# Performance work log

Hardware: AMD Instinct MI355X
Metric: run time of the kernel (lower is better)

The kernel has to match this reference:

```python
import jax, jax.numpy as jnp
import numpy as np

B, IN, OUT, STY = 8192, 2048, 2048, 512

def setup_inputs() -> dict:
    key = jax.random.key(0)
    k1, k2, k3, k4, k5 = jax.random.split(key, 5)
    bound_w = 1.0 / np.sqrt(IN)  # kaiming_uniform(a=sqrt(5)) on (OUT,IN) -> U(-1/sqrt(IN), 1/sqrt(IN))
    weight = jax.random.uniform(k1, (OUT, IN), jnp.float32, -bound_w, bound_w)
    bias = jax.random.uniform(k2, (OUT,), jnp.float32, -bound_w, bound_w)
    bound_a = 1.0 / np.sqrt(STY)
    aff_w = jax.random.uniform(k3, (2 * OUT, STY), jnp.float32, -bound_a, bound_a)
    aff_b = jnp.concatenate([jnp.ones((OUT,), jnp.float32), jnp.zeros((OUT,), jnp.float32)])
    inp = jax.random.normal(k4, (B, IN), jnp.float32)
    style = jax.random.normal(k5, (B, STY), jnp.float32)
    return {"input": inp, "style": style, "weight": weight, "bias": bias,
            "aff_w": aff_w, "aff_b": aff_b}

def reference(input, style, weight, bias, aff_w, aff_b):
    # affine: (B, 2*OUT), chunk into scale / (unused) style-bias
    enc = style @ aff_w.T + aff_b
    scale = enc[:, :OUT]  # (B, OUT); second chunk is discarded by the original forward
    # Original math: w1 = W * s[b,o]; norm = rsqrt(sum_i w1^2); w2 = w1 / norm = w1 * sqrt(sum_i w1^2)
    # sum_i (W[o,i]*s[b,o])^2 = s[b,o]^2 * rowsq[o]  ->  w2[b,o,i] = W[o,i] * s*|s| * sqrt(rowsq[o])
    rowsq = jnp.sum(weight * weight, axis=1)                  # (OUT,)
    mod = scale * jnp.abs(scale) * jnp.sqrt(rowsq)[None, :]   # (B, OUT)
    base = input @ weight.T                                   # (B, OUT) single GEMM
    return base * mod + bias[None, :]
```

## Files before the change

kernel.cpp:

```cpp
#include <hip/hip_runtime.h>
#include <cstdint>
#include <cstddef>

#define B_ROWS 8192
#define IN_DIM 2048
#define OUT_DIM 2048
#define STY_DIM 512

typedef unsigned short u16;
typedef __attribute__((ext_vector_type(8))) short bf16x8;
typedef __attribute__((ext_vector_type(4))) float f32x4;

__device__ __forceinline__ void cvt_pair(float x0, float x1, uint32_t& hi, uint32_t& lo) {
  uint32_t u0 = __float_as_uint(x0), u1 = __float_as_uint(x1);
  uint32_t a0 = u0 & 0xffff0000u, a1 = u1 & 0xffff0000u;
  hi = (u0 >> 16) | a1;
  float l0 = x0 - __uint_as_float(a0);
  float l1 = x1 - __uint_as_float(a1);
  lo = (__float_as_uint(l0) >> 16) | (__float_as_uint(l1) & 0xffff0000u);
}


__global__ void split_kernel(const float* __restrict__ src,
                             u16* __restrict__ hi, u16* __restrict__ lo, int n4) {
  int stride = gridDim.x * blockDim.x;
  for (int i = blockIdx.x * blockDim.x + threadIdx.x; i < n4; i += stride) {
    float4 v = reinterpret_cast<const float4*>(src)[i];
    uint32_t h0, h1, l0, l1;
    cvt_pair(v.x, v.y, h0, l0);
    cvt_pair(v.z, v.w, h1, l1);
    uint2 hw; hw.x = h0; hw.y = h1;
    uint2 lw; lw.x = l0; lw.y = l1;
    reinterpret_cast<uint2*>(hi)[i] = hw;
    reinterpret_cast<uint2*>(lo)[i] = lw;
  }
}

__global__ void rowsq_kernel(const float* __restrict__ w, float* __restrict__ srq) {
  int row  = blockIdx.x * 4 + (threadIdx.x >> 6);
  int lane = threadIdx.x & 63;
  const float4* p = reinterpret_cast<const float4*>(w + (size_t)row * IN_DIM);
  float s = 0.f;
  #pragma unroll
  for (int i = 0; i < 8; ++i) {
    float4 v = p[lane + i * 64];
    s += v.x * v.x + v.y * v.y + v.z * v.z + v.w * v.w;
  }
  #pragma unroll
  for (int off = 32; off > 0; off >>= 1) s += __shfl_down(s, off);
  if (lane == 0) srq[row] = sqrtf(s);
}

template<int LDK, int NT>
__device__ __forceinline__ void gemm_bf16_phase(
    const u16* __restrict__ gAhi, const u16* __restrict__ gAlo,
    const u16* __restrict__ gBhi, const u16* __restrict__ gBlo,
    f32x4 (&acc)[4][4],
    u16* sAhi, u16* sAlo, u16* sBhi, u16* sBlo,
    int tid)
{
  const int lane = tid & 63;
  const int wid  = tid >> 6;
  const int wr = wid >> 1, wc = wid & 1;
  const int fr = lane & 15, kg = lane >> 4;

  const u16* gsrc = (wid == 0) ? gAhi : (wid == 1) ? gAlo : (wid == 2) ? gBhi : gBlo;
  u16* sdst = (wid == 0) ? sAhi : (wid == 1) ? sAlo : (wid == 2) ? sBhi : sBlo;
  const u16* gl = gsrc + (size_t)(lane >> 2) * LDK + (size_t)(lane & 3) * 8;

  const int aoff = (wr * 64 + fr) * 32 + kg * 8;
  const int boff = (wc * 64 + fr) * 32 + kg * 8;

  for (int t = 0; t < NT; ++t) {
    __syncthreads();
    {
      const u16* g = gl + t * 32;
      #pragma unroll
      for (int i = 0; i < 8; ++i) {
        __builtin_amdgcn_global_load_lds(
            (const __attribute__((address_space(1))) void*)(g),
            (__attribute__((address_space(3))) void*)(sdst + i * 512),
            16, 0, 0);
        g += (size_t)16 * LDK;
      }
    }
    __syncthreads();

    bf16x8 bh[4], bl[4];
    #pragma unroll
    for (int nj = 0; nj < 4; ++nj) {
      bh[nj] = *reinterpret_cast<const bf16x8*>(sBhi + boff + nj * 16 * 32);
      bl[nj] = *reinterpret_cast<const bf16x8*>(sBlo + boff + nj * 16 * 32);
    }
    #pragma unroll
    for (int mi = 0; mi < 4; ++mi) {
      bf16x8 ah = *reinterpret_cast<const bf16x8*>(sAhi + aoff + mi * 16 * 32);
      bf16x8 al = *reinterpret_cast<const bf16x8*>(sAlo + aoff + mi * 16 * 32);
      #pragma unroll
      for (int nj = 0; nj < 4; ++nj) {
        acc[mi][nj] = __builtin_amdgcn_mfma_f32_16x16x32_bf16(ah, bh[nj], acc[mi][nj], 0, 0, 0);
        acc[mi][nj] = __builtin_amdgcn_mfma_f32_16x16x32_bf16(ah, bl[nj], acc[mi][nj], 0, 0, 0);
        acc[mi][nj] = __builtin_amdgcn_mfma_f32_16x16x32_bf16(al, bh[nj], acc[mi][nj], 0, 0, 0);
      }
    }
  }
}

__global__ __launch_bounds__(256, 2) void fused_fast(
    const u16* __restrict__ ihi, const u16* __restrict__ ilo,
    const u16* __restrict__ whi, const u16* __restrict__ wlo,
    const u16* __restrict__ shi, const u16* __restrict__ slo,
    const u16* __restrict__ awhi, const u16* __restrict__ awlo,
    const float* __restrict__ bias, const float* __restrict__ aff_b,
    const float* __restrict__ srq, float* __restrict__ out)
{
  __shared__ u16 sAhi[128 * 32];
  __shared__ u16 sAlo[128 * 32];
  __shared__ u16 sBhi[128 * 32];
  __shared__ u16 sBlo[128 * 32];

  const int tid = threadIdx.x;
  const int bn = blockIdx.x, bm = blockIdx.y;
  const int brow = bm * 128, bcol = bn * 128;
  const int lane = tid & 63, wid = tid >> 6;
  const int wr = wid >> 1, wc = wid & 1;
  const int fr = lane & 15, kg = lane >> 4;

  f32x4 sacc[4][4];
  #pragma unroll
  for (int i = 0; i < 4; ++i)
    #pragma unroll
    for (int j = 0; j < 4; ++j) {
      f32x4 z = {0.f, 0.f, 0.f, 0.f};
      sacc[i][j] = z;
    }

  gemm_bf16_phase<STY_DIM, STY_DIM / 32>(
      shi + (size_t)brow * STY_DIM, slo + (size_t)brow * STY_DIM,
      awhi + (size_t)bcol * STY_DIM, awlo + (size_t)bcol * STY_DIM,
      sacc, sAhi, sAlo, sBhi, sBlo, tid);

  float affb[4], srqv[4], biasv[4];
  #pragma unroll
  for (int nj = 0; nj < 4; ++nj) {
    int c = bcol + wc * 64 + nj * 16 + fr;
    affb[nj]  = aff_b[c];
    srqv[nj]  = srq[c];
    biasv[nj] = bias[c];
  }

  #pragma unroll
  for (int mi = 0; mi < 4; ++mi)
    #pragma unroll
    for (int nj = 0; nj < 4; ++nj)
      #pragma unroll
      for (int r = 0; r < 4; ++r) {
        float s = sacc[mi][nj][r] + affb[nj];
        sacc[mi][nj][r] = s * fabsf(s) * srqv[nj];
      }

  f32x4 acc[4][4];
  #pragma unroll
  for (int i = 0; i < 4; ++i)
    #pragma unroll
    for (int j = 0; j < 4; ++j) {
      f32x4 z = {0.f, 0.f, 0.f, 0.f};
      acc[i][j] = z;
    }

  gemm_bf16_phase<IN_DIM, IN_DIM / 32>(
      ihi + (size_t)brow * IN_DIM, ilo + (size_t)brow * IN_DIM,
      whi + (size_t)bcol * IN_DIM, wlo + (size_t)bcol * IN_DIM,
      acc, sAhi, sAlo, sBhi, sBlo, tid);

  #pragma unroll
  for (int mi = 0; mi < 4; ++mi) {
    int r0 = brow + wr * 64 + mi * 16 + kg * 4;
    #pragma unroll
    for (int nj = 0; nj < 4; ++nj) {
      int c = bcol + wc * 64 + nj * 16 + fr;
      float* po = out + (size_t)r0 * OUT_DIM + c;
      #pragma unroll
      for (int r = 0; r < 4; ++r) {
        po[(size_t)r * OUT_DIM] = acc[mi][nj][r] * sacc[mi][nj][r] + biasv[nj];
      }
    }
  }
}


#define BMf 128
#define BNf 128
#define BKf 32
#define PAD_K 40

__device__ __forceinline__ void write_rep(const float4& v, u16* baseHi, u16* baseLo) {
  uint32_t h0, h1, l0, l1;
  cvt_pair(v.x, v.y, h0, l0);
  cvt_pair(v.z, v.w, h1, l1);
  uint2 hw; hw.x = h0; hw.y = h1;
  uint2 lw; lw.x = l0; lw.y = l1;
  *reinterpret_cast<uint2*>(baseHi) = hw;
  *reinterpret_cast<uint2*>(baseLo) = lw;
}

template<int LDK, int NT>
__device__ __forceinline__ void gemm_phase(
    const float* __restrict__ gA, const float* __restrict__ gB,
    f32x4 (&acc)[4][4],
    u16* sAhi, u16* sAlo, u16* sBhi, u16* sBlo,
    int tid)
{
  const int sr = tid >> 3;
  const int sk = (tid & 7) * 4;
  const float* pa = gA + (size_t)sr * LDK + sk;
  const float* pb = gB + (size_t)sr * LDK + sk;
  const int lbase = sr * PAD_K + sk;

  const int lane = tid & 63;
  const int wid  = tid >> 6;
  const int wr = wid >> 1, wc = wid & 1;
  const int fr = lane & 15;
  const int kg = lane >> 4;
  const int aoff = (wr * 64 + fr) * PAD_K + kg * 8;
  const int boff = (wc * 64 + fr) * PAD_K + kg * 8;

  float4 va[4], vb[4];
  #pragma unroll
  for (int rep = 0; rep < 4; ++rep) {
    va[rep] = *reinterpret_cast<const float4*>(pa + (size_t)rep * 32 * LDK);
    vb[rep] = *reinterpret_cast<const float4*>(pb + (size_t)rep * 32 * LDK);
  }
  pa += BKf; pb += BKf;

  for (int t = 0; t < NT; ++t) {
    __syncthreads();
    #pragma unroll
    for (int rep = 0; rep < 4; ++rep) {
      write_rep(va[rep], sAhi + lbase + rep * 32 * PAD_K, sAlo + lbase + rep * 32 * PAD_K);
      write_rep(vb[rep], sBhi + lbase + rep * 32 * PAD_K, sBlo + lbase + rep * 32 * PAD_K);
    }
    __syncthreads();
    if (t + 1 < NT) {
      #pragma unroll
      for (int rep = 0; rep < 4; ++rep) {
        va[rep] = *reinterpret_cast<const float4*>(pa + (size_t)rep * 32 * LDK);
        vb[rep] = *reinterpret_cast<const float4*>(pb + (size_t)rep * 32 * LDK);
      }
      pa += BKf; pb += BKf;
    }

    bf16x8 bhi[4], blo[4];
    #pragma unroll
    for (int nj = 0; nj < 4; ++nj) {
      bhi[nj] = *reinterpret_cast<const bf16x8*>(sBhi + boff + nj * 16 * PAD_K);
      blo[nj] = *reinterpret_cast<const bf16x8*>(sBlo + boff + nj * 16 * PAD_K);
    }
    #pragma unroll
    for (int mi = 0; mi < 4; ++mi) {
      bf16x8 ahi = *reinterpret_cast<const bf16x8*>(sAhi + aoff + mi * 16 * PAD_K);
      bf16x8 alo = *reinterpret_cast<const bf16x8*>(sAlo + aoff + mi * 16 * PAD_K);
      #pragma unroll
      for (int nj = 0; nj < 4; ++nj) {
        acc[mi][nj] = __builtin_amdgcn_mfma_f32_16x16x32_bf16(ahi, bhi[nj], acc[mi][nj], 0, 0, 0);
        acc[mi][nj] = __builtin_amdgcn_mfma_f32_16x16x32_bf16(ahi, blo[nj], acc[mi][nj], 0, 0, 0);
        acc[mi][nj] = __builtin_amdgcn_mfma_f32_16x16x32_bf16(alo, bhi[nj], acc[mi][nj], 0, 0, 0);
      }
    }
  }
  __syncthreads();
}

__global__ __launch_bounds__(256, 2) void fused_style_linear(
    const float* __restrict__ input, const float* __restrict__ style,
    const float* __restrict__ weight, const float* __restrict__ bias,
    const float* __restrict__ aff_w, const float* __restrict__ aff_b,
    const float* __restrict__ srq, float* __restrict__ out)
{
  __shared__ u16 sAhi[BMf * PAD_K];
  __shared__ u16 sAlo[BMf * PAD_K];
  __shared__ u16 sBhi[BNf * PAD_K];
  __shared__ u16 sBlo[BNf * PAD_K];

  const int tid = threadIdx.x;
  const int bn = blockIdx.x, bm = blockIdx.y;
  const int brow = bm * BMf, bcol = bn * BNf;

  const int lane = tid & 63, wid = tid >> 6;
  const int wr = wid >> 1, wc = wid & 1;
  const int fr = lane & 15, kg = lane >> 4;

  f32x4 sacc[4][4];
  #pragma unroll
  for (int i = 0; i < 4; ++i)
    #pragma unroll
    for (int j = 0; j < 4; ++j) {
      f32x4 z = {0.f, 0.f, 0.f, 0.f};
      sacc[i][j] = z;
    }

  gemm_phase<STY_DIM, STY_DIM / BKf>(style + (size_t)brow * STY_DIM,
                                     aff_w + (size_t)bcol * STY_DIM,
                                     sacc, sAhi, sAlo, sBhi, sBlo, tid);

  float affb[4], srqv[4], biasv[4];
  #pragma unroll
  for (int nj = 0; nj < 4; ++nj) {
    int c = bcol + wc * 64 + nj * 16 + fr;
    affb[nj]  = aff_b[c];
    srqv[nj]  = srq[c];
    biasv[nj] = bias[c];
  }

  #pragma unroll
  for (int mi = 0; mi < 4; ++mi)
    #pragma unroll
    for (int nj = 0; nj < 4; ++nj)
      #pragma unroll
      for (int r = 0; r < 4; ++r) {
        float s = sacc[mi][nj][r] + affb[nj];
        sacc[mi][nj][r] = s * fabsf(s) * srqv[nj];
      }

  f32x4 acc[4][4];
  #pragma unroll
  for (int i = 0; i < 4; ++i)
    #pragma unroll
    for (int j = 0; j < 4; ++j) {
      f32x4 z = {0.f, 0.f, 0.f, 0.f};
      acc[i][j] = z;
    }

  gemm_phase<IN_DIM, IN_DIM / BKf>(input + (size_t)brow * IN_DIM,
                                   weight + (size_t)bcol * IN_DIM,
                                   acc, sAhi, sAlo, sBhi, sBlo, tid);

  #pragma unroll
  for (int mi = 0; mi < 4; ++mi) {
    int r0 = brow + wr * 64 + mi * 16 + kg * 4;
    #pragma unroll
    for (int nj = 0; nj < 4; ++nj) {
      int c = bcol + wc * 64 + nj * 16 + fr;
      float* po = out + (size_t)r0 * OUT_DIM + c;
      #pragma unroll
      for (int r = 0; r < 4; ++r) {
        po[(size_t)r * OUT_DIM] = acc[mi][nj][r] * sacc[mi][nj][r] + biasv[nj];
      }
    }
  }
}


extern "C" void kernel_launch(void* const* d_in, const int* in_sizes, int n_in,
                              void* d_out, int out_size, void* d_ws, size_t ws_size,
                              hipStream_t stream) {
  (void)in_sizes; (void)n_in; (void)out_size;
  const float* input  = (const float*)d_in[0];
  const float* style  = (const float*)d_in[1];
  const float* weight = (const float*)d_in[2];
  const float* bias   = (const float*)d_in[3];
  const float* aff_w  = (const float*)d_in[4];
  const float* aff_b  = (const float*)d_in[5];
  float* out = (float*)d_out;

  const size_t OFF_IHI = 0;
  const size_t OFF_ILO = OFF_IHI + (size_t)B_ROWS * IN_DIM * 2;
  const size_t OFF_WHI = OFF_ILO + (size_t)B_ROWS * IN_DIM * 2;
  const size_t OFF_WLO = OFF_WHI + (size_t)OUT_DIM * IN_DIM * 2;
  const size_t OFF_SHI = OFF_WLO + (size_t)OUT_DIM * IN_DIM * 2;
  const size_t OFF_SLO = OFF_SHI + (size_t)B_ROWS * STY_DIM * 2;
  const size_t OFF_AHI = OFF_SLO + (size_t)B_ROWS * STY_DIM * 2;
  const size_t OFF_ALO = OFF_AHI + (size_t)OUT_DIM * STY_DIM * 2;
  const size_t OFF_SRQ = OFF_ALO + (size_t)OUT_DIM * STY_DIM * 2;
  const size_t WS_NEEDED = OFF_SRQ + OUT_DIM * 4;

  if (ws_size >= WS_NEEDED) {
    char* ws = (char*)d_ws;
    u16* ihi = (u16*)(ws + OFF_IHI);
    u16* ilo = (u16*)(ws + OFF_ILO);
    u16* whi = (u16*)(ws + OFF_WHI);
    u16* wlo = (u16*)(ws + OFF_WLO);
    u16* shi = (u16*)(ws + OFF_SHI);
    u16* slo = (u16*)(ws + OFF_SLO);
    u16* awhi = (u16*)(ws + OFF_AHI);
    u16* awlo = (u16*)(ws + OFF_ALO);
    float* srq = (float*)(ws + OFF_SRQ);

    split_kernel<<<2048, 256, 0, stream>>>(input,  ihi,  ilo,  B_ROWS * IN_DIM / 4);
    split_kernel<<<2048, 256, 0, stream>>>(weight, whi,  wlo,  OUT_DIM * IN_DIM / 4);
    split_kernel<<<2048, 256, 0, stream>>>(style,  shi,  slo,  B_ROWS * STY_DIM / 4);
    split_kernel<<<1024, 256, 0, stream>>>(aff_w,  awhi, awlo, OUT_DIM * STY_DIM / 4);
    rowsq_kernel<<<OUT_DIM / 4, 256, 0, stream>>>(weight, srq);

    dim3 grid(OUT_DIM / 128, B_ROWS / 128);
    fused_fast<<<grid, 256, 0, stream>>>(ihi, ilo, whi, wlo, shi, slo, awhi, awlo,
                                         bias, aff_b, srq, out);
  } else {
    float* srq = (float*)d_ws;
    rowsq_kernel<<<OUT_DIM / 4, 256, 0, stream>>>(weight, srq);
    dim3 grid(OUT_DIM / BNf, B_ROWS / BMf);
    fused_style_linear<<<grid, 256, 0, stream>>>(input, style, weight, bias,
                                                 aff_w, aff_b, srq, out);
  }
}
```

Baseline: 393.7 us.

## Merge split and rowsq kernels, swizzle LDS layout, raise GEMM occupancy

The four split kernels and the row-norm kernel become one launch, and the weight split computes row sums of squares in the same pass, so weight is read once and launch overhead drops. The GEMM phase XOR-swizzles the 16-byte k-chunks in LDS on both the global-to-LDS copy and the fragment reads, to reduce bank conflicts. Launch bounds on fused_fast go from 2 to 4 blocks per CU, which limits registers per thread and may cause spills with the large accumulator array.

```diff
diff --git a/kernel.cpp b/kernel.cpp
--- a/kernel.cpp
+++ b/kernel.cpp
@@ -20,35 +20,63 @@
   lo = (__float_as_uint(l0) >> 16) | (__float_as_uint(l1) & 0xffff0000u);
 }
 
-
-__global__ void split_kernel(const float* __restrict__ src,
-                             u16* __restrict__ hi, u16* __restrict__ lo, int n4) {
-  int stride = gridDim.x * blockDim.x;
-  for (int i = blockIdx.x * blockDim.x + threadIdx.x; i < n4; i += stride) {
-    float4 v = reinterpret_cast<const float4*>(src)[i];
-    uint32_t h0, h1, l0, l1;
-    cvt_pair(v.x, v.y, h0, l0);
-    cvt_pair(v.z, v.w, h1, l1);
-    uint2 hw; hw.x = h0; hw.y = h1;
-    uint2 lw; lw.x = l0; lw.y = l1;
-    reinterpret_cast<uint2*>(hi)[i] = hw;
-    reinterpret_cast<uint2*>(lo)[i] = lw;
-  }
-}
-
-__global__ void rowsq_kernel(const float* __restrict__ w, float* __restrict__ srq) {
-  int row  = blockIdx.x * 4 + (threadIdx.x >> 6);
-  int lane = threadIdx.x & 63;
-  const float4* p = reinterpret_cast<const float4*>(w + (size_t)row * IN_DIM);
-  float s = 0.f;
-  #pragma unroll
-  for (int i = 0; i < 8; ++i) {
-    float4 v = p[lane + i * 64];
-    s += v.x * v.x + v.y * v.y + v.z * v.z + v.w * v.w;
-  }
-  #pragma unroll
-  for (int off = 32; off > 0; off >>= 1) s += __shfl_down(s, off);
-  if (lane == 0) srq[row] = sqrtf(s);
+__device__ __forceinline__ void split_one(const float* __restrict__ src,
+                                          u16* __restrict__ hi, u16* __restrict__ lo, int i) {
+  float4 v = reinterpret_cast<const float4*>(src)[i];
+  uint32_t h0, h1, l0, l1;
+  cvt_pair(v.x, v.y, h0, l0);
+  cvt_pair(v.z, v.w, h1, l1);
+  uint2 hw; hw.x = h0; hw.y = h1;
+  uint2 lw; lw.x = l0; lw.y = l1;
+  reinterpret_cast<uint2*>(hi)[i] = hw;
+  reinterpret_cast<uint2*>(lo)[i] = lw;
+}
+
+
+__global__ __launch_bounds__(256) void split_all(
+    const float* __restrict__ input, const float* __restrict__ weight,
+    const float* __restrict__ style, const float* __restrict__ aff_w,
+    u16* __restrict__ ihi, u16* __restrict__ ilo,
+    u16* __restrict__ whi, u16* __restrict__ wlo,
+    u16* __restrict__ shi, u16* __restrict__ slo,
+    u16* __restrict__ awhi, u16* __restrict__ awlo,
+    float* __restrict__ srq)
+{
+  const int b = blockIdx.x, tid = threadIdx.x;
+  if (b < 2048) {
+    int i = b * 256 + tid;
+    #pragma unroll
+    for (int k = 0; k < 8; ++k) { split_one(input, ihi, ilo, i); i += 2048 * 256; }
+  } else if (b < 2560) {
+    int row  = (b - 2048) * 4 + (tid >> 6);
+    int lane = tid & 63;
+    const float4* p = reinterpret_cast<const float4*>(weight) + (size_t)row * (IN_DIM / 4);
+    float s = 0.f;
+    #pragma unroll
+    for (int k = 0; k < 8; ++k) {
+      int i = lane + k * 64;
+      float4 v = p[i];
+      s += v.x * v.x + v.y * v.y + v.z * v.z + v.w * v.w;
+      uint32_t h0, h1, l0, l1;
+      cvt_pair(v.x, v.y, h0, l0);
+      cvt_pair(v.z, v.w, h1, l1);
+      uint2 hw; hw.x = h0; hw.y = h1;
+      uint2 lw; lw.x = l0; lw.y = l1;
+      reinterpret_cast<uint2*>(whi)[(size_t)row * (IN_DIM / 4) + i] = hw;
+      reinterpret_cast<uint2*>(wlo)[(size_t)row * (IN_DIM / 4) + i] = lw;
+    }
+    #pragma unroll
+    for (int off = 32; off > 0; off >>= 1) s += __shfl_down(s, off);
+    if (lane == 0) srq[row] = sqrtf(s);
+  } else if (b < 3072) {
+    int i = (b - 2560) * 256 + tid;
+    #pragma unroll
+    for (int k = 0; k < 8; ++k) { split_one(style, shi, slo, i); i += 512 * 256; }
+  } else {
+    int i = (b - 3072) * 256 + tid;
+    #pragma unroll
+    for (int k = 0; k < 16; ++k) { split_one(aff_w, awhi, awlo, i); i += 64 * 256; }
+  }
 }
 
 template<int LDK, int NT>
@@ -66,10 +94,12 @@
 
   const u16* gsrc = (wid == 0) ? gAhi : (wid == 1) ? gAlo : (wid == 2) ? gBhi : gBlo;
   u16* sdst = (wid == 0) ? sAhi : (wid == 1) ? sAlo : (wid == 2) ? sBhi : sBlo;
-  const u16* gl = gsrc + (size_t)(lane >> 2) * LDK + (size_t)(lane & 3) * 8;
-
-  const int aoff = (wr * 64 + fr) * 32 + kg * 8;
-  const int boff = (wc * 64 + fr) * 32 + kg * 8;
+  const int src_chunk = (lane & 3) ^ ((lane >> 3) & 3);
+  const u16* gl = gsrc + (size_t)(lane >> 2) * LDK + (size_t)src_chunk * 8;
+
+  const int kswz = (kg ^ ((fr >> 1) & 3)) * 8;
+  const int aoff = (wr * 64 + fr) * 32 + kswz;
+  const int boff = (wc * 64 + fr) * 32 + kswz;
 
   for (int t = 0; t < NT; ++t) {
     __syncthreads();
@@ -106,7 +136,7 @@
   }
 }
 
-__global__ __launch_bounds__(256, 2) void fused_fast(
+__global__ __launch_bounds__(256, 4) void fused_fast(
     const u16* __restrict__ ihi, const u16* __restrict__ ilo,
     const u16* __restrict__ whi, const u16* __restrict__ wlo,
     const u16* __restrict__ shi, const u16* __restrict__ slo,
@@ -271,6 +301,21 @@
   __syncthreads();
 }
 
+__global__ void rowsq_kernel(const float* __restrict__ w, float* __restrict__ srq) {
+  int row  = blockIdx.x * 4 + (threadIdx.x >> 6);
+  int lane = threadIdx.x & 63;
+  const float4* p = reinterpret_cast<const float4*>(w + (size_t)row * IN_DIM);
+  float s = 0.f;
+  #pragma unroll
+  for (int i = 0; i < 8; ++i) {
+    float4 v = p[lane + i * 64];
+    s += v.x * v.x + v.y * v.y + v.z * v.z + v.w * v.w;
+  }
+  #pragma unroll
+  for (int off = 32; off > 0; off >>= 1) s += __shfl_down(s, off);
+  if (lane == 0) srq[row] = sqrtf(s);
+}
+
 __global__ __launch_bounds__(256, 2) void fused_style_linear(
     const float* __restrict__ input, const float* __restrict__ style,
     const float* __restrict__ weight, const float* __restrict__ bias,
@@ -386,11 +431,8 @@
     u16* awlo = (u16*)(ws + OFF_ALO);
     float* srq = (float*)(ws + OFF_SRQ);
 
-    split_kernel<<<2048, 256, 0, stream>>>(input,  ihi,  ilo,  B_ROWS * IN_DIM / 4);
-    split_kernel<<<2048, 256, 0, stream>>>(weight, whi,  wlo,  OUT_DIM * IN_DIM / 4);
-    split_kernel<<<2048, 256, 0, stream>>>(style,  shi,  slo,  B_ROWS * STY_DIM / 4);
-    split_kernel<<<1024, 256, 0, stream>>>(aff_w,  awhi, awlo, OUT_DIM * STY_DIM / 4);
-    rowsq_kernel<<<OUT_DIM / 4, 256, 0, stream>>>(weight, srq);
+    split_all<<<3136, 256, 0, stream>>>(input, weight, style, aff_w,
+                                        ihi, ilo, whi, wlo, shi, slo, awhi, awlo, srq);
 
     dim3 grid(OUT_DIM / 128, B_ROWS / 128);
     fused_fast<<<grid, 256, 0, stream>>>(ihi, ilo, whi, wlo, shi, slo, awhi, awlo,
```

Measured after the change: 957.6 us. +143.2%, slower.
